# Performance work log

Measured on AMD Instinct MI355X. Metric: run time of the kernel, lower is better.

## Reference

```python
import jax, jax.numpy as jnp
import numpy as np

N, IN, HID, HEADS, FFN = 2048, 768, 1024, 8, 2048
NH = HID // HEADS  # 128 per-head hidden


def setup_inputs() -> dict:
    key = jax.random.key(0)
    ks = jax.random.split(key, 24)
    s = 0.02
    inp = {
        "feature": jax.random.normal(ks[0], (1, N, IN), jnp.float32),
        "adj": jax.random.bernoulli(ks[1], 0.05, (1, N, N)).astype(jnp.float32),
        "gat1_W1": jax.random.normal(ks[2], (IN, HID), jnp.float32) * s,
        "gat1_a1": jax.random.normal(ks[3], (2 * NH,), jnp.float32) * s,
        "gat1_W2": jax.random.normal(ks[4], (HID, IN), jnp.float32) * s,
        "gat1_a2": jax.random.normal(ks[5], (2 * IN,), jnp.float32) * s,
        "gat2_W1": jax.random.normal(ks[6], (IN, HID), jnp.float32) * s,
        "gat2_a1": jax.random.normal(ks[7], (2 * NH,), jnp.float32) * s,
        "gat2_W2": jax.random.normal(ks[8], (HID, IN), jnp.float32) * s,
        "gat2_a2": jax.random.normal(ks[9], (2 * IN,), jnp.float32) * s,
        "Wf": jax.random.normal(ks[10], (2 * IN, IN), jnp.float32) * s,
        "bf": jnp.zeros((IN,), jnp.float32),
        "ffn_W1": jax.random.normal(ks[11], (IN, FFN), jnp.float32) * s,
        "ffn_b1": jnp.zeros((FFN,), jnp.float32),
        "ffn_W2": jax.random.normal(ks[12], (FFN, FFN), jnp.float32) * s,
        "ffn_b2": jnp.zeros((FFN,), jnp.float32),
        "ffn_W3": jax.random.normal(ks[13], (FFN, IN), jnp.float32) * s,
        "ffn_b3": jnp.zeros((IN,), jnp.float32),
        "out_W1": jax.random.normal(ks[14], (IN, FFN), jnp.float32) * s,
        "out_b1": jnp.zeros((FFN,), jnp.float32),
        "out_W2": jax.random.normal(ks[15], (FFN, IN), jnp.float32) * s,
        "out_b2": jnp.zeros((IN,), jnp.float32),
    }
    return inp


def leaky(x, slope):
    return jnp.where(x >= 0, x, slope * x)


def gat_layer(h, adjb, W, a, heads, concat):
    # h: [N, F_in]; adjb: [N, N] bool. Scores decompose since attn weight is
    # shared across heads: e_ij = leaky(a_l . g_i + a_r . g_j).
    n = h.shape[0]
    g = (h @ W).reshape(n, heads, -1)           # [N, H, F']
    f = g.shape[-1]
    gl = jnp.einsum("nhf,f->nh", g, a[:f])
    gr = jnp.einsum("nhf,f->nh", g, a[f:])
    e = leaky(gl[:, None, :] + gr[None, :, :], 0.2)   # [N, N, H]
    e = jnp.where(adjb[:, :, None], e, jnp.float32(-1e9))
    att = jax.nn.softmax(e, axis=1)             # softmax over source j
    out = jnp.einsum("ijh,jhf->ihf", att, g)    # [N, H, F']
    return out.reshape(n, -1) if concat else out.mean(axis=1)


def gat(x, adj2d, W1, a1, W2, a2):
    adjb = adj2d != 0
    x1 = jax.nn.elu(gat_layer(x, adjb, W1, a1, HEADS, True))
    return gat_layer(x1, adjb, W2, a2, 1, False)


def reference(feature, adj, gat1_W1, gat1_a1, gat1_W2, gat1_a2,
              gat2_W1, gat2_a1, gat2_W2, gat2_a2, Wf, bf,
              ffn_W1, ffn_b1, ffn_W2, ffn_b2, ffn_W3, ffn_b3,
              out_W1, out_b1, out_W2, out_b2):
    sen_adj = adj.at[:, :, -6:].set(0.0)
    sec_adj = jnp.zeros_like(adj).at[:, :, -6:].set(adj[:, :, -6:])
    x = feature[0]                               # [N, IN]
    f_sen = gat(x, sen_adj[0], gat1_W1, gat1_a1, gat1_W2, gat1_a2) + x
    f_sec = gat(x, sec_adj[0], gat2_W1, gat2_a1, gat2_W2, gat2_a2) + x
    f = jnp.concatenate([f_sec, f_sen], axis=-1)
    f = leaky(f @ Wf + bf, 0.01)                 # fusion linear + leaky
    # ffn: MLP(layers=3, keep_last=False) -> act on every layer
    f = leaky(f @ ffn_W1 + ffn_b1, 0.01)
    f = leaky(f @ ffn_W2 + ffn_b2, 0.01)
    f = leaky(f @ ffn_W3 + ffn_b3, 0.01)
    # out_ffn: MLP(layers=2)
    o = leaky(f @ out_W1 + out_b1, 0.01)
    o = leaky(o @ out_W2 + out_b2, 0.01)
    return (o + x)[None]                         # residual, [1, N, IN]
```

## Files before the change

### kernel.cpp

```cpp
#include <hip/hip_runtime.h>
#include <hip/hip_bf16.h>
#include <cmath>

#define NN 2048
#define DIN 768
#define DHID 1024
#define NHEADS 8
#define FPRIME 128
#define DFFN 2048
#define SEN_LIM 2042
#define MAXDEG 256

using short8 = __attribute__((ext_vector_type(8))) short;
using f32x4  = __attribute__((ext_vector_type(4))) float;

#if defined(__has_builtin)
#  if __has_builtin(__builtin_amdgcn_global_load_lds)
#    define HAVE_GLL 1
#  endif
#endif
#ifndef HAVE_GLL
#  define HAVE_GLL 0
#endif

__device__ inline unsigned short f2bf(float f) {
    unsigned u = __float_as_uint(f);
    unsigned r = u + 0x7FFFu + ((u >> 16) & 1u);
    return (unsigned short)(r >> 16);
}
__device__ inline float bf2f(unsigned short h) {
    return __uint_as_float(((unsigned)h) << 16);
}
__device__ inline void store_out(float* p, float v) { *p = v; }
__device__ inline void store_out(unsigned short* p, float v) { *p = f2bf(v); }

#if HAVE_GLL
__device__ inline void gll16(const unsigned short* g, unsigned short* l) {
    __builtin_amdgcn_global_load_lds(
        (const __attribute__((address_space(1))) unsigned int*)g,
        (__attribute__((address_space(3))) unsigned int*)l, 16, 0, 0);
}
#endif

__global__ __launch_bounds__(256) void build_nbrs(
    const float* __restrict__ adj,
    unsigned short* __restrict__ sen_idx, int* __restrict__ sen_cnt,
    unsigned short* __restrict__ sec_idx, int* __restrict__ sec_cnt)
{
    const int i = blockIdx.x;
    __shared__ int c_sen, c_sec;
    if (threadIdx.x == 0) { c_sen = 0; c_sec = 0; }
    __syncthreads();
    for (int j4 = threadIdx.x; j4 < NN / 4; j4 += 256) {
        float4 v = *(const float4*)&adj[(size_t)i * NN + j4 * 4];
        float vs[4] = {v.x, v.y, v.z, v.w};
        #pragma unroll
        for (int q = 0; q < 4; ++q) {
            if (vs[q] != 0.0f) {
                int j = j4 * 4 + q;
                if (j < SEN_LIM) {
                    int p = atomicAdd(&c_sen, 1);
                    if (p < MAXDEG) sen_idx[(size_t)i * MAXDEG + p] = (unsigned short)j;
                } else {
                    int p = atomicAdd(&c_sec, 1);
                    if (p < 8) sec_idx[i * 8 + p] = (unsigned short)j;
                }
            }
        }
    }
    __syncthreads();
    if (threadIdx.x == 0) { sen_cnt[i] = min(c_sen, MAXDEG); sec_cnt[i] = min(c_sec, 8); }
}

__global__ __launch_bounds__(256) void transpose_cast(
    const float* __restrict__ W, unsigned short* __restrict__ WT, int K, int N)
{
    __shared__ float t[32][33];
    const int bn = blockIdx.x * 32, bk = blockIdx.y * 32;
    const int tx = threadIdx.x & 31, ty = threadIdx.x >> 5;
    #pragma unroll
    for (int r = 0; r < 4; ++r)
        t[ty + r * 8][tx] = W[(size_t)(bk + ty + r * 8) * N + bn + tx];
    __syncthreads();
    #pragma unroll
    for (int r = 0; r < 4; ++r) {
        int n = ty + r * 8;
        WT[(size_t)(bn + n) * K + bk + tx] = f2bf(t[tx][n]);
    }
}

__global__ __launch_bounds__(256) void cast_bf16(
    const float* __restrict__ in, unsigned short* __restrict__ out, int n)
{
    int t = blockIdx.x * 256 + threadIdx.x;
    if (t < n) out[t] = f2bf(in[t]);
}

__global__ __launch_bounds__(256) void zero_f32(float* p, int n)
{
    int t = blockIdx.x * 256 + threadIdx.x;
    if (t < n) p[t] = 0.f;
}

__global__ __launch_bounds__(256) void col_mean(
    const float* __restrict__ g, int C, float* __restrict__ out)
{
    int c = blockIdx.x * 256 + threadIdx.x;
    int r0 = blockIdx.y * 128;
    float s = 0.f;
    for (int r = r0; r < r0 + 128; ++r) s += g[(size_t)r * C + c];
    atomicAdd(&out[c], s * (1.0f / 2048.0f));
}

template<int BM, int BN, typename OUT_T>
__global__ __launch_bounds__(256) void gemm_mfma(
    const unsigned short* __restrict__ A, const unsigned short* __restrict__ BT,
    const float* __restrict__ bias, const float* __restrict__ resid,
    OUT_T* __restrict__ C, unsigned short* __restrict__ Cb,
    int M, int N, int K, int act)
{
    constexpr int BK = 64;
    constexpr int WR = BM / 64;
    constexpr int WC = 4 / WR;
    constexpr int NF = BN / (WC * 16);
    constexpr int ACH = BM / 32;
    constexpr int BCH = BN / 32;
    __shared__ unsigned short Asm[BM * BK];
    __shared__ unsigned short Bsm[BN * BK];
    const int tid = threadIdx.x;
    const int lane = tid & 63, w = tid >> 6;
    const int wr = w / WC, wc = w % WC;
    const int bm = blockIdx.y * BM, bn = blockIdx.x * BN;

    f32x4 acc[4][NF];
    #pragma unroll
    for (int mi = 0; mi < 4; ++mi)
        #pragma unroll
        for (int ni = 0; ni < NF; ++ni)
            acc[mi][ni] = (f32x4){0.f, 0.f, 0.f, 0.f};

    const unsigned short* Abase = A + (size_t)bm * K;
    const unsigned short* Bbase = BT + (size_t)bn * K;

    for (int k0 = 0; k0 < K; k0 += BK) {
        __syncthreads();
        #pragma unroll
        for (int c = 0; c < ACH; ++c) {
            int e = (tid + c * 256) * 8;
            int r = e >> 6, kk = e & 63;
            int kks = kk ^ ((r & 7) << 3);
#if HAVE_GLL
            gll16(&Abase[(size_t)r * K + k0 + kks], &Asm[e]);
#else
            *(short8*)&Asm[e] = *(const short8*)&Abase[(size_t)r * K + k0 + kks];
#endif
        }
        #pragma unroll
        for (int c = 0; c < BCH; ++c) {
            int e = (tid + c * 256) * 8;
            int r = e >> 6, kk = e & 63;
            int kks = kk ^ ((r & 7) << 3);
#if HAVE_GLL
            gll16(&Bbase[(size_t)r * K + k0 + kks], &Bsm[e]);
#else
            *(short8*)&Bsm[e] = *(const short8*)&Bbase[(size_t)r * K + k0 + kks];
#endif
        }
        __syncthreads();
        #pragma unroll
        for (int ks = 0; ks < 2; ++ks) {
            short8 af[4], bfv[NF];
            #pragma unroll
            for (int mi = 0; mi < 4; ++mi) {
                int row = wr * 64 + mi * 16 + (lane & 15);
                int col = (ks * 32 + (lane >> 4) * 8) ^ ((row & 7) << 3);
                af[mi] = *(const short8*)&Asm[row * 64 + col];
            }
            #pragma unroll
            for (int ni = 0; ni < NF; ++ni) {
                int row = wc * (BN / WC) + ni * 16 + (lane & 15);
                int col = (ks * 32 + (lane >> 4) * 8) ^ ((row & 7) << 3);
                bfv[ni] = *(const short8*)&Bsm[row * 64 + col];
            }
            #pragma unroll
            for (int mi = 0; mi < 4; ++mi)
                #pragma unroll
                for (int ni = 0; ni < NF; ++ni)
                    acc[mi][ni] = __builtin_amdgcn_mfma_f32_16x16x32_bf16(
                        af[mi], bfv[ni], acc[mi][ni], 0, 0, 0);
        }
    }

    const int rbase = bm + wr * 64;
    const int cbase = bn + wc * (BN / WC);
    #pragma unroll
    for (int mi = 0; mi < 4; ++mi)
        #pragma unroll
        for (int ni = 0; ni < NF; ++ni)
            #pragma unroll
            for (int r = 0; r < 4; ++r) {
                int grow = rbase + mi * 16 + (lane >> 4) * 4 + r;
                int gcol = cbase + ni * 16 + (lane & 15);
                float v = acc[mi][ni][r];
                if (bias)  v += bias[gcol];
                if (act)   v = (v >= 0.f) ? v : 0.01f * v;
                if (resid) v += resid[(size_t)grow * N + gcol];
                store_out(&C[(size_t)grow * N + gcol], v);
                if (Cb) Cb[(size_t)grow * N + gcol] = f2bf(v);
            }
}

__global__ __launch_bounds__(64) void glgr_kernel(
    const float* __restrict__ g, const float* __restrict__ a,
    int F, float* __restrict__ gl, float* __restrict__ gr)
{
    const int b = blockIdx.x;
    const int lane = threadIdx.x;
    const float* gb = g + (size_t)b * F;
    float sl = 0.f, sr = 0.f;
    for (int f = lane; f < F; f += 64) {
        float v = gb[f];
        sl += v * a[f];
        sr += v * a[F + f];
    }
    #pragma unroll
    for (int off = 32; off > 0; off >>= 1) {
        sl += __shfl_down(sl, off);
        sr += __shfl_down(sr, off);
    }
    if (lane == 0) { gl[b] = sl; gr[b] = sr; }
}

template<int H, int F, typename OUT_T>
__global__ __launch_bounds__(256) void attn_agg(
    const float* __restrict__ g,
    const unsigned short* __restrict__ gb,
    const float* __restrict__ gl,
    const float* __restrict__ gr,
    const unsigned short* __restrict__ idx, int idx_stride,
    const int* __restrict__ cnt,
    const float* __restrict__ gmean,
    OUT_T* __restrict__ dst, int dst_stride, int dst_coloff,
    const float* __restrict__ resid, int mode)
{
    constexpr int HF = H * F;
    const int i = blockIdx.x;
    const int tid = threadIdx.x;
    const int lane = tid & 63, w = tid >> 6;
    const int n = cnt[i];

    if (n == 0) {
        for (int c = tid; c < HF; c += 256) {
            float v = gmean[c];
            if (mode == 0) v = (v > 0.f) ? v : expm1f(v);
            else           v += resid[(size_t)i * HF + c];
            store_out(&dst[(size_t)i * dst_stride + dst_coloff + c], v);
        }
        return;
    }

    __shared__ float s_wred[4 * H];
    __shared__ float s_max[H], s_inv[H], s_glh[H];
    __shared__ float s_w[128 * H];
    __shared__ unsigned short s_j[128];

    if (tid < H) s_glh[tid] = gl[(size_t)i * H + tid];
    __syncthreads();
    float glh[H];
    #pragma unroll
    for (int h = 0; h < H; ++h) glh[h] = s_glh[h];

    const unsigned short* row_idx = idx + (size_t)i * idx_stride;

    float pmax[H];
    #pragma unroll
    for (int h = 0; h < H; ++h) pmax[h] = -1e30f;
    for (int jj = tid; jj < n; jj += 256) {
        int j = row_idx[jj];
        if (H == 8) {
            float4 ga = *(const float4*)&gr[(size_t)j * 8];
            float4 gbv = *(const float4*)&gr[(size_t)j * 8 + 4];
            float sc[8] = {ga.x, ga.y, ga.z, ga.w, gbv.x, gbv.y, gbv.z, gbv.w};
            #pragma unroll
            for (int h = 0; h < H; ++h) {
                float s = glh[h] + sc[h];
                s = (s >= 0.f) ? s : 0.2f * s;
                pmax[h] = fmaxf(pmax[h], s);
            }
        } else {
            float s = glh[0] + gr[j];
            s = (s >= 0.f) ? s : 0.2f * s;
            pmax[0] = fmaxf(pmax[0], s);
        }
    }
    #pragma unroll
    for (int h = 0; h < H; ++h)
        #pragma unroll
        for (int off = 32; off > 0; off >>= 1)
            pmax[h] = fmaxf(pmax[h], __shfl_xor(pmax[h], off));
    if (lane == 0)
        #pragma unroll
        for (int h = 0; h < H; ++h) s_wred[w * H + h] = pmax[h];
    __syncthreads();
    if (tid < H)
        s_max[tid] = fmaxf(fmaxf(s_wred[tid], s_wred[H + tid]),
                           fmaxf(s_wred[2 * H + tid], s_wred[3 * H + tid]));
    __syncthreads();
    float mx[H];
    #pragma unroll
    for (int h = 0; h < H; ++h) mx[h] = s_max[h];

    float psum[H];
    #pragma unroll
    for (int h = 0; h < H; ++h) psum[h] = 0.f;
    for (int jj = tid; jj < n; jj += 256) {
        int j = row_idx[jj];
        if (H == 8) {
            float4 ga = *(const float4*)&gr[(size_t)j * 8];
            float4 gbv = *(const float4*)&gr[(size_t)j * 8 + 4];
            float sc[8] = {ga.x, ga.y, ga.z, ga.w, gbv.x, gbv.y, gbv.z, gbv.w};
            #pragma unroll
            for (int h = 0; h < H; ++h) {
                float s = glh[h] + sc[h];
                s = (s >= 0.f) ? s : 0.2f * s;
                psum[h] += expf(s - mx[h]);
            }
        } else {
            float s = glh[0] + gr[j];
            s = (s >= 0.f) ? s : 0.2f * s;
            psum[0] += expf(s - mx[0]);
        }
    }
    #pragma unroll
    for (int h = 0; h < H; ++h)
        #pragma unroll
        for (int off = 32; off > 0; off >>= 1)
            psum[h] += __shfl_xor(psum[h], off);
    if (lane == 0)
        #pragma unroll
        for (int h = 0; h < H; ++h) s_wred[w * H + h] = psum[h];
    __syncthreads();
    if (tid < H)
        s_inv[tid] = 1.f / (s_wred[tid] + s_wred[H + tid] +
                            s_wred[2 * H + tid] + s_wred[3 * H + tid]);

    const int cb = tid * 4;
    const bool active = (cb < HF);
    const int hh = (H == 8) ? (cb >> 7) : 0;
    float a0 = 0.f, a1 = 0.f, a2 = 0.f, a3 = 0.f;

    for (int c0 = 0; c0 < n; c0 += 128) {
        int m = min(128, n - c0);
        __syncthreads();
        for (int e = tid; e < m * H; e += 256) {
            int jj = (H == 8) ? (e >> 3) : e;
            int h  = (H == 8) ? (e & 7) : 0;
            int j = row_idx[c0 + jj];
            float s = glh[h] + gr[(size_t)j * H + h];
            s = (s >= 0.f) ? s : 0.2f * s;
            s_w[jj * H + h] = expf(s - s_max[h]) * s_inv[h];
            if (h == 0) s_j[jj] = (unsigned short)j;
        }
        __syncthreads();
        if (active) {
            int jj = 0;
            for (; jj + 4 <= m; jj += 4) {
                ushort4 v0 = *(const ushort4*)&gb[(size_t)s_j[jj]     * HF + cb];
                ushort4 v1 = *(const ushort4*)&gb[(size_t)s_j[jj + 1] * HF + cb];
                ushort4 v2 = *(const ushort4*)&gb[(size_t)s_j[jj + 2] * HF + cb];
                ushort4 v3 = *(const ushort4*)&gb[(size_t)s_j[jj + 3] * HF + cb];
                float w0 = s_w[jj * H + hh], w1 = s_w[(jj + 1) * H + hh];
                float w2 = s_w[(jj + 2) * H + hh], w3 = s_w[(jj + 3) * H + hh];
                a0 += w0 * bf2f(v0.x) + w1 * bf2f(v1.x) + w2 * bf2f(v2.x) + w3 * bf2f(v3.x);
                a1 += w0 * bf2f(v0.y) + w1 * bf2f(v1.y) + w2 * bf2f(v2.y) + w3 * bf2f(v3.y);
                a2 += w0 * bf2f(v0.z) + w1 * bf2f(v1.z) + w2 * bf2f(v2.z) + w3 * bf2f(v3.z);
                a3 += w0 * bf2f(v0.w) + w1 * bf2f(v1.w) + w2 * bf2f(v2.w) + w3 * bf2f(v3.w);
            }
            for (; jj < m; ++jj) {
                ushort4 v0 = *(const ushort4*)&gb[(size_t)s_j[jj] * HF + cb];
                float w0 = s_w[jj * H + hh];
                a0 += w0 * bf2f(v0.x); a1 += w0 * bf2f(v0.y);
                a2 += w0 * bf2f(v0.z); a3 += w0 * bf2f(v0.w);
            }
        }
    }

    if (active) {
        float vv[4] = {a0, a1, a2, a3};
        #pragma unroll
        for (int q = 0; q < 4; ++q) {
            float v = vv[q];
            if (mode == 0) v = (v > 0.f) ? v : expm1f(v);
            else           v += resid[(size_t)i * HF + cb + q];
            store_out(&dst[(size_t)i * dst_stride + dst_coloff + cb + q], v);
        }
    }
}

extern "C" void kernel_launch(void* const* d_in, const int* in_sizes, int n_in,
                              void* d_out, int out_size, void* d_ws, size_t ws_size,
                              hipStream_t stream)
{
    const float* feature = (const float*)d_in[0];
    const float* adj     = (const float*)d_in[1];
    const float* g1W1 = (const float*)d_in[2];
    const float* g1a1 = (const float*)d_in[3];
    const float* g1W2 = (const float*)d_in[4];
    const float* g1a2 = (const float*)d_in[5];
    const float* g2W1 = (const float*)d_in[6];
    const float* g2a1 = (const float*)d_in[7];
    const float* g2W2 = (const float*)d_in[8];
    const float* g2a2 = (const float*)d_in[9];
    const float* Wf  = (const float*)d_in[10];
    const float* bfv = (const float*)d_in[11];
    const float* fW1 = (const float*)d_in[12];
    const float* fb1 = (const float*)d_in[13];
    const float* fW2 = (const float*)d_in[14];
    const float* fb2 = (const float*)d_in[15];
    const float* fW3 = (const float*)d_in[16];
    const float* fb3 = (const float*)d_in[17];
    const float* oW1 = (const float*)d_in[18];
    const float* ob1 = (const float*)d_in[19];
    const float* oW2 = (const float*)d_in[20];
    const float* ob2 = (const float*)d_in[21];
    float* out = (float*)d_out;

    char* ws = (char*)d_ws;
    size_t off = 0;
    auto alloc = [&](size_t bytes) -> void* {
        void* p = ws + off;
        off = (off + bytes + 255) & ~(size_t)255;
        return p;
    };
    typedef unsigned short bf_t;
    int* sen_cnt = (int*)alloc((size_t)NN * 4);
    int* sec_cnt = (int*)alloc((size_t)NN * 4);
    unsigned short* sen_idx = (unsigned short*)alloc((size_t)NN * MAXDEG * 2);
    unsigned short* sec_idx = (unsigned short*)alloc((size_t)NN * 8 * 2);
    float* g1buf = (float*)alloc((size_t)NN * DHID * 4);
    bf_t*  g1b   = (bf_t*)alloc((size_t)NN * DHID * 2);
    float* gl1   = (float*)alloc((size_t)NN * NHEADS * 4);
    float* gr1   = (float*)alloc((size_t)NN * NHEADS * 4);
    bf_t*  x1    = (bf_t*)alloc((size_t)NN * DHID * 2);
    float* g2buf = (float*)alloc((size_t)NN * DIN * 4);
    bf_t*  g2b   = (bf_t*)alloc((size_t)NN * DIN * 2);
    float* gl2   = (float*)alloc((size_t)NN * 4);
    float* gr2   = (float*)alloc((size_t)NN * 4);
    float* gmean = (float*)alloc((size_t)DHID * 4);
    bf_t*  fcat  = (bf_t*)alloc((size_t)NN * (2 * DIN) * 2);
    bf_t*  fbuf  = (bf_t*)alloc((size_t)NN * DIN * 2);
    bf_t*  tA    = (bf_t*)alloc((size_t)NN * DFFN * 2);
    bf_t*  tB    = (bf_t*)alloc((size_t)NN * DFFN * 2);
    bf_t*  featb = (bf_t*)alloc((size_t)NN * DIN * 2);
    bf_t* g1W1T = (bf_t*)alloc((size_t)DIN * DHID * 2);
    bf_t* g1W2T = (bf_t*)alloc((size_t)DHID * DIN * 2);
    bf_t* g2W1T = (bf_t*)alloc((size_t)DIN * DHID * 2);
    bf_t* g2W2T = (bf_t*)alloc((size_t)DHID * DIN * 2);
    bf_t* WfT   = (bf_t*)alloc((size_t)(2 * DIN) * DIN * 2);
    bf_t* fW1T  = (bf_t*)alloc((size_t)DIN * DFFN * 2);
    bf_t* fW2T  = (bf_t*)alloc((size_t)DFFN * DFFN * 2);
    bf_t* fW3T  = (bf_t*)alloc((size_t)DFFN * DIN * 2);
    bf_t* oW1T  = (bf_t*)alloc((size_t)DIN * DFFN * 2);
    bf_t* oW2T  = (bf_t*)alloc((size_t)DFFN * DIN * 2);

    build_nbrs<<<NN, 256, 0, stream>>>(adj, sen_idx, sen_cnt, sec_idx, sec_cnt);
    auto tp = [&](const float* W, bf_t* WT, int K, int N) {
        transpose_cast<<<dim3(N / 32, K / 32), 256, 0, stream>>>(W, WT, K, N);
    };
    tp(g1W1, g1W1T, DIN, DHID);   tp(g1W2, g1W2T, DHID, DIN);
    tp(g2W1, g2W1T, DIN, DHID);   tp(g2W2, g2W2T, DHID, DIN);
    tp(Wf, WfT, 2 * DIN, DIN);
    tp(fW1, fW1T, DIN, DFFN);     tp(fW2, fW2T, DFFN, DFFN);
    tp(fW3, fW3T, DFFN, DIN);
    tp(oW1, oW1T, DIN, DFFN);     tp(oW2, oW2T, DFFN, DIN);
    cast_bf16<<<(NN * DIN) / 256, 256, 0, stream>>>(feature, featb, NN * DIN);

    auto run_gat = [&](const bf_t* W1T, const float* a1, const bf_t* W2T, const float* a2,
                       const unsigned short* idx, int idx_stride, const int* cnt, int coloff) {
        gemm_mfma<64, 64, float><<<dim3(DHID / 64, NN / 64), 256, 0, stream>>>(
            featb, W1T, nullptr, nullptr, g1buf, g1b, NN, DHID, DIN, 0);
        glgr_kernel<<<NN * NHEADS, 64, 0, stream>>>(g1buf, a1, FPRIME, gl1, gr1);
        zero_f32<<<DHID / 256, 256, 0, stream>>>(gmean, DHID);
        col_mean<<<dim3(DHID / 256, 16), 256, 0, stream>>>(g1buf, DHID, gmean);
        attn_agg<NHEADS, FPRIME, bf_t><<<NN, 256, 0, stream>>>(
            g1buf, g1b, gl1, gr1, idx, idx_stride, cnt, gmean, x1, DHID, 0, nullptr, 0);
        gemm_mfma<64, 64, float><<<dim3(DIN / 64, NN / 64), 256, 0, stream>>>(
            x1, W2T, nullptr, nullptr, g2buf, g2b, NN, DIN, DHID, 0);
        glgr_kernel<<<NN, 64, 0, stream>>>(g2buf, a2, DIN, gl2, gr2);
        zero_f32<<<DIN / 256, 256, 0, stream>>>(gmean, DIN);
        col_mean<<<dim3(DIN / 256, 16), 256, 0, stream>>>(g2buf, DIN, gmean);
        attn_agg<1, DIN, bf_t><<<NN, 256, 0, stream>>>(
            g2buf, g2b, gl2, gr2, idx, idx_stride, cnt, gmean, fcat, 2 * DIN, coloff, feature, 1);
    };

    run_gat(g1W1T, g1a1, g1W2T, g1a2, sen_idx, MAXDEG, sen_cnt, DIN);
    run_gat(g2W1T, g2a1, g2W2T, g2a2, sec_idx, 8, sec_cnt, 0);

    gemm_mfma<64, 64, bf_t><<<dim3(DIN / 64, NN / 64), 256, 0, stream>>>(
        fcat, WfT, bfv, nullptr, fbuf, nullptr, NN, DIN, 2 * DIN, 1);
    gemm_mfma<64, 128, bf_t><<<dim3(DFFN / 128, NN / 64), 256, 0, stream>>>(
        fbuf, fW1T, fb1, nullptr, tA, nullptr, NN, DFFN, DIN, 1);
    gemm_mfma<64, 128, bf_t><<<dim3(DFFN / 128, NN / 64), 256, 0, stream>>>(
        tA, fW2T, fb2, nullptr, tB, nullptr, NN, DFFN, DFFN, 1);
    gemm_mfma<64, 64, bf_t><<<dim3(DIN / 64, NN / 64), 256, 0, stream>>>(
        tB, fW3T, fb3, nullptr, fbuf, nullptr, NN, DIN, DFFN, 1);
    gemm_mfma<64, 128, bf_t><<<dim3(DFFN / 128, NN / 64), 256, 0, stream>>>(
        fbuf, oW1T, ob1, nullptr, tA, nullptr, NN, DFFN, DIN, 1);
    gemm_mfma<64, 64, float><<<dim3(DIN / 64, NN / 64), 256, 0, stream>>>(
        tA, oW2T, ob2, feature, out, nullptr, NN, DIN, DFFN, 1);
}
```

Before: 522.2 us.

## Batch both GAT branches into shared launches and merge weight preprocessing

Merges all weight transposes and the feature cast into a single job-table kernel. It concatenates the two first-layer GAT weights into one wider GEMM, and runs the second-layer GEMM, score, column-mean and aggregation kernels for both branches in one launch each via a branch index. Intermediate projections are kept in bf16 only, which removes the fp32 copies and halves traffic for scores and means. The aggregation inner loop is unrolled to 8 neighbors. The aim is to cut launch count and fill the GPU better for the tiny second branch, at the cost of reading scores and means from bf16-rounded values.

```diff
diff --git a/kernel.cpp b/kernel.cpp
--- a/kernel.cpp
+++ b/kernel.cpp
@@ -72,51 +72,47 @@
     if (threadIdx.x == 0) { sen_cnt[i] = min(c_sen, MAXDEG); sec_cnt[i] = min(c_sec, 8); }
 }
 
-__global__ __launch_bounds__(256) void transpose_cast(
-    const float* __restrict__ W, unsigned short* __restrict__ WT, int K, int N)
+struct TPJob { const float* s; unsigned short* d; int K, N, start, trans; };
+struct TPJobs { TPJob j[11]; };
+
+__global__ __launch_bounds__(256) void mega_tp(TPJobs jobs, int njobs)
 {
     __shared__ float t[32][33];
-    const int bn = blockIdx.x * 32, bk = blockIdx.y * 32;
+    const int tile = blockIdx.x;
+    int ji = 0;
+    for (int k = 1; k < 11; ++k)
+        if (k < njobs && tile >= jobs.j[k].start) ji = k;
+    const TPJob jb = jobs.j[ji];
+    const int lt = tile - jb.start;
+    const int ntx = jb.N >> 5;
+    const int bn = (lt % ntx) * 32, bk = (lt / ntx) * 32;
     const int tx = threadIdx.x & 31, ty = threadIdx.x >> 5;
-    #pragma unroll
-    for (int r = 0; r < 4; ++r)
-        t[ty + r * 8][tx] = W[(size_t)(bk + ty + r * 8) * N + bn + tx];
-    __syncthreads();
-    #pragma unroll
-    for (int r = 0; r < 4; ++r) {
-        int n = ty + r * 8;
-        WT[(size_t)(bn + n) * K + bk + tx] = f2bf(t[tx][n]);
-    }
-}
-
-__global__ __launch_bounds__(256) void cast_bf16(
-    const float* __restrict__ in, unsigned short* __restrict__ out, int n)
-{
-    int t = blockIdx.x * 256 + threadIdx.x;
-    if (t < n) out[t] = f2bf(in[t]);
-}
-
-__global__ __launch_bounds__(256) void zero_f32(float* p, int n)
-{
-    int t = blockIdx.x * 256 + threadIdx.x;
-    if (t < n) p[t] = 0.f;
-}
-
-__global__ __launch_bounds__(256) void col_mean(
-    const float* __restrict__ g, int C, float* __restrict__ out)
-{
-    int c = blockIdx.x * 256 + threadIdx.x;
-    int r0 = blockIdx.y * 128;
-    float s = 0.f;
-    for (int r = r0; r < r0 + 128; ++r) s += g[(size_t)r * C + c];
-    atomicAdd(&out[c], s * (1.0f / 2048.0f));
+    if (jb.trans) {
+        #pragma unroll
+        for (int r = 0; r < 4; ++r)
+            t[ty + r * 8][tx] = jb.s[(size_t)(bk + ty + r * 8) * jb.N + bn + tx];
+        __syncthreads();
+        #pragma unroll
+        for (int r = 0; r < 4; ++r) {
+            int n = ty + r * 8;
+            jb.d[(size_t)(bn + n) * jb.K + bk + tx] = f2bf(t[tx][n]);
+        }
+    } else {
+        #pragma unroll
+        for (int r = 0; r < 4; ++r) {
+            size_t e = (size_t)(bk + ty + r * 8) * jb.N + bn + tx;
+            jb.d[e] = f2bf(jb.s[e]);
+        }
+    }
 }
 
 template<int BM, int BN, typename OUT_T>
 __global__ __launch_bounds__(256) void gemm_mfma(
-    const unsigned short* __restrict__ A, const unsigned short* __restrict__ BT,
+    const unsigned short* __restrict__ A0, const unsigned short* __restrict__ A1,
+    const unsigned short* __restrict__ BT0, const unsigned short* __restrict__ BT1,
     const float* __restrict__ bias, const float* __restrict__ resid,
-    OUT_T* __restrict__ C, unsigned short* __restrict__ Cb,
+    OUT_T* __restrict__ C0, OUT_T* __restrict__ C1,
+    unsigned short* __restrict__ Cb0, unsigned short* __restrict__ Cb1,
     int M, int N, int K, int act)
 {
     constexpr int BK = 64;
@@ -127,6 +123,11 @@
     constexpr int BCH = BN / 32;
     __shared__ unsigned short Asm[BM * BK];
     __shared__ unsigned short Bsm[BN * BK];
+    const int z = blockIdx.z;
+    const unsigned short* A  = z ? A1  : A0;
+    const unsigned short* BT = z ? BT1 : BT0;
+    OUT_T* C = z ? C1 : C0;
+    unsigned short* Cb = z ? Cb1 : Cb0;
     const int tid = threadIdx.x;
     const int lane = tid & 63, w = tid >> 6;
     const int wr = w / WC, wc = w % WC;
@@ -210,16 +211,24 @@
             }
 }
 
-__global__ __launch_bounds__(64) void glgr_kernel(
-    const float* __restrict__ g, const float* __restrict__ a,
-    int F, float* __restrict__ gl, float* __restrict__ gr)
-{
-    const int b = blockIdx.x;
-    const int lane = threadIdx.x;
-    const float* gb = g + (size_t)b * F;
+__global__ __launch_bounds__(64) void glgr2(
+    const unsigned short* __restrict__ gA, const unsigned short* __restrict__ gB,
+    int row_stride, int F, int Hlog2, int nb_per_branch,
+    const float* __restrict__ aA, const float* __restrict__ aB,
+    float* __restrict__ glA, float* __restrict__ grA,
+    float* __restrict__ glB, float* __restrict__ grB,
+    float* __restrict__ z, int zblocks)
+{
+    const int bid = blockIdx.x, lane = threadIdx.x;
+    if (bid < zblocks) z[bid * 64 + lane] = 0.f;
+    const int br = bid >= nb_per_branch;
+    const int b = br ? bid - nb_per_branch : bid;
+    const int node = b >> Hlog2, h = b - ((b >> Hlog2) << Hlog2);
+    const unsigned short* g = (br ? gB : gA) + (size_t)node * row_stride + h * F;
+    const float* a = br ? aB : aA;
     float sl = 0.f, sr = 0.f;
     for (int f = lane; f < F; f += 64) {
-        float v = gb[f];
+        float v = bf2f(g[f]);
         sl += v * a[f];
         sr += v * a[F + f];
     }
@@ -228,23 +237,52 @@
         sl += __shfl_down(sl, off);
         sr += __shfl_down(sr, off);
     }
-    if (lane == 0) { gl[b] = sl; gr[b] = sr; }
+    if (lane == 0) {
+        (br ? glB : glA)[b] = sl;
+        (br ? grB : grA)[b] = sr;
+    }
+}
+
+__global__ __launch_bounds__(256) void col_mean2(
+    const unsigned short* __restrict__ g0, const unsigned short* __restrict__ g1,
+    int C, float* __restrict__ o0, float* __restrict__ o1)
+{
+    const unsigned short* g = blockIdx.z ? g1 : g0;
+    float* o = blockIdx.z ? o1 : o0;
+    int c = blockIdx.x * 256 + threadIdx.x;
+    int r0 = blockIdx.y * 128;
+    float s = 0.f;
+    for (int r = r0; r < r0 + 128; ++r) s += bf2f(g[(size_t)r * C + c]);
+    atomicAdd(&o[c], s * (1.0f / 2048.0f));
 }
 
 template<int H, int F, typename OUT_T>
-__global__ __launch_bounds__(256) void attn_agg(
-    const float* __restrict__ g,
-    const unsigned short* __restrict__ gb,
-    const float* __restrict__ gl,
-    const float* __restrict__ gr,
-    const unsigned short* __restrict__ idx, int idx_stride,
-    const int* __restrict__ cnt,
-    const float* __restrict__ gmean,
-    OUT_T* __restrict__ dst, int dst_stride, int dst_coloff,
+__global__ __launch_bounds__(256) void attn_agg2(
+    const unsigned short* __restrict__ gb0, const unsigned short* __restrict__ gb1,
+    int g_stride,
+    const float* __restrict__ gl0, const float* __restrict__ gr0,
+    const float* __restrict__ gl1, const float* __restrict__ gr1,
+    const unsigned short* __restrict__ idx0, int is0, const int* __restrict__ cnt0,
+    const unsigned short* __restrict__ idx1, int is1, const int* __restrict__ cnt1,
+    const float* __restrict__ gmean0, const float* __restrict__ gmean1,
+    OUT_T* __restrict__ dst0, OUT_T* __restrict__ dst1,
+    int dst_stride, int co0, int co1,
     const float* __restrict__ resid, int mode)
 {
     constexpr int HF = H * F;
-    const int i = blockIdx.x;
+    const int bid = blockIdx.x;
+    const int br = bid >= NN;
+    const int i = br ? bid - NN : bid;
+    const unsigned short* gbp = br ? gb1 : gb0;
+    const float* gl = br ? gl1 : gl0;
+    const float* gr = br ? gr1 : gr0;
+    const unsigned short* idx = br ? idx1 : idx0;
+    const int is = br ? is1 : is0;
+    const int* cnt = br ? cnt1 : cnt0;
+    const float* gmean = br ? gmean1 : gmean0;
+    OUT_T* dst = br ? dst1 : dst0;
+    const int co = br ? co1 : co0;
+
     const int tid = threadIdx.x;
     const int lane = tid & 63, w = tid >> 6;
     const int n = cnt[i];
@@ -254,7 +292,7 @@
             float v = gmean[c];
             if (mode == 0) v = (v > 0.f) ? v : expm1f(v);
             else           v += resid[(size_t)i * HF + c];
-            store_out(&dst[(size_t)i * dst_stride + dst_coloff + c], v);
+            store_out(&dst[(size_t)i * dst_stride + co + c], v);
         }
         return;
     }
@@ -270,7 +308,7 @@
     #pragma unroll
     for (int h = 0; h < H; ++h) glh[h] = s_glh[h];
 
-    const unsigned short* row_idx = idx + (size_t)i * idx_stride;
+    const unsigned short* row_idx = idx + (size_t)i * is;
 
     float pmax[H];
     #pragma unroll
@@ -364,20 +402,23 @@
         __syncthreads();
         if (active) {
             int jj = 0;
-            for (; jj + 4 <= m; jj += 4) {
-                ushort4 v0 = *(const ushort4*)&gb[(size_t)s_j[jj]     * HF + cb];
-                ushort4 v1 = *(const ushort4*)&gb[(size_t)s_j[jj + 1] * HF + cb];
-                ushort4 v2 = *(const ushort4*)&gb[(size_t)s_j[jj + 2] * HF + cb];
-                ushort4 v3 = *(const ushort4*)&gb[(size_t)s_j[jj + 3] * HF + cb];
-                float w0 = s_w[jj * H + hh], w1 = s_w[(jj + 1) * H + hh];
-                float w2 = s_w[(jj + 2) * H + hh], w3 = s_w[(jj + 3) * H + hh];
-                a0 += w0 * bf2f(v0.x) + w1 * bf2f(v1.x) + w2 * bf2f(v2.x) + w3 * bf2f(v3.x);
-                a1 += w0 * bf2f(v0.y) + w1 * bf2f(v1.y) + w2 * bf2f(v2.y) + w3 * bf2f(v3.y);
-                a2 += w0 * bf2f(v0.z) + w1 * bf2f(v1.z) + w2 * bf2f(v2.z) + w3 * bf2f(v3.z);
-                a3 += w0 * bf2f(v0.w) + w1 * bf2f(v1.w) + w2 * bf2f(v2.w) + w3 * bf2f(v3.w);
+            for (; jj + 8 <= m; jj += 8) {
+                ushort4 v[8]; float wv[8];
+                #pragma unroll
+                for (int u = 0; u < 8; ++u) {
+                    v[u] = *(const ushort4*)&gbp[(size_t)s_j[jj + u] * g_stride + cb];
+                    wv[u] = s_w[(jj + u) * H + hh];
+                }
+                #pragma unroll
+                for (int u = 0; u < 8; ++u) {
+                    a0 += wv[u] * bf2f(v[u].x);
+                    a1 += wv[u] * bf2f(v[u].y);
+                    a2 += wv[u] * bf2f(v[u].z);
+                    a3 += wv[u] * bf2f(v[u].w);
+                }
             }
             for (; jj < m; ++jj) {
-                ushort4 v0 = *(const ushort4*)&gb[(size_t)s_j[jj] * HF + cb];
+                ushort4 v0 = *(const ushort4*)&gbp[(size_t)s_j[jj] * g_stride + cb];
                 float w0 = s_w[jj * H + hh];
                 a0 += w0 * bf2f(v0.x); a1 += w0 * bf2f(v0.y);
                 a2 += w0 * bf2f(v0.z); a3 += w0 * bf2f(v0.w);
@@ -392,7 +433,7 @@
             float v = vv[q];
             if (mode == 0) v = (v > 0.f) ? v : expm1f(v);
             else           v += resid[(size_t)i * HF + cb + q];
-            store_out(&dst[(size_t)i * dst_stride + dst_coloff + cb + q], v);
+            store_out(&dst[(size_t)i * dst_stride + co + cb + q], v);
         }
     }
 }
@@ -437,24 +478,28 @@
     int* sec_cnt = (int*)alloc((size_t)NN * 4);
     unsigned short* sen_idx = (unsigned short*)alloc((size_t)NN * MAXDEG * 2);
     unsigned short* sec_idx = (unsigned short*)alloc((size_t)NN * 8 * 2);
-    float* g1buf = (float*)alloc((size_t)NN * DHID * 4);
-    bf_t*  g1b   = (bf_t*)alloc((size_t)NN * DHID * 2);
-    float* gl1   = (float*)alloc((size_t)NN * NHEADS * 4);
-    float* gr1   = (float*)alloc((size_t)NN * NHEADS * 4);
-    bf_t*  x1    = (bf_t*)alloc((size_t)NN * DHID * 2);
-    float* g2buf = (float*)alloc((size_t)NN * DIN * 4);
-    bf_t*  g2b   = (bf_t*)alloc((size_t)NN * DIN * 2);
-    float* gl2   = (float*)alloc((size_t)NN * 4);
-    float* gr2   = (float*)alloc((size_t)NN * 4);
-    float* gmean = (float*)alloc((size_t)DHID * 4);
+    bf_t*  g1b   = (bf_t*)alloc((size_t)NN * 2048 * 2);
+    float* gl1a  = (float*)alloc((size_t)NN * NHEADS * 4);
+    float* gr1a  = (float*)alloc((size_t)NN * NHEADS * 4);
+    float* gl1b  = (float*)alloc((size_t)NN * NHEADS * 4);
+    float* gr1b  = (float*)alloc((size_t)NN * NHEADS * 4);
+    bf_t*  x1a   = (bf_t*)alloc((size_t)NN * DHID * 2);
+    bf_t*  x1b   = (bf_t*)alloc((size_t)NN * DHID * 2);
+    bf_t*  g2aB  = (bf_t*)alloc((size_t)NN * DIN * 2);
+    bf_t*  g2bB  = (bf_t*)alloc((size_t)NN * DIN * 2);
+    float* gl2a  = (float*)alloc((size_t)NN * 4);
+    float* gr2a  = (float*)alloc((size_t)NN * 4);
+    float* gl2b  = (float*)alloc((size_t)NN * 4);
+    float* gr2b  = (float*)alloc((size_t)NN * 4);
+    float* gmeanL1 = (float*)alloc((size_t)2048 * 4);
+    float* gmeanL2 = (float*)alloc((size_t)1536 * 4);
     bf_t*  fcat  = (bf_t*)alloc((size_t)NN * (2 * DIN) * 2);
     bf_t*  fbuf  = (bf_t*)alloc((size_t)NN * DIN * 2);
     bf_t*  tA    = (bf_t*)alloc((size_t)NN * DFFN * 2);
     bf_t*  tB    = (bf_t*)alloc((size_t)NN * DFFN * 2);
     bf_t*  featb = (bf_t*)alloc((size_t)NN * DIN * 2);
-    bf_t* g1W1T = (bf_t*)alloc((size_t)DIN * DHID * 2);
+    bf_t* W1T_AB = (bf_t*)alloc((size_t)2048 * DIN * 2);
     bf_t* g1W2T = (bf_t*)alloc((size_t)DHID * DIN * 2);
-    bf_t* g2W1T = (bf_t*)alloc((size_t)DIN * DHID * 2);
     bf_t* g2W2T = (bf_t*)alloc((size_t)DHID * DIN * 2);
     bf_t* WfT   = (bf_t*)alloc((size_t)(2 * DIN) * DIN * 2);
     bf_t* fW1T  = (bf_t*)alloc((size_t)DIN * DFFN * 2);
@@ -464,48 +509,75 @@
     bf_t* oW2T  = (bf_t*)alloc((size_t)DFFN * DIN * 2);
 
     build_nbrs<<<NN, 256, 0, stream>>>(adj, sen_idx, sen_cnt, sec_idx, sec_cnt);
-    auto tp = [&](const float* W, bf_t* WT, int K, int N) {
-        transpose_cast<<<dim3(N / 32, K / 32), 256, 0, stream>>>(W, WT, K, N);
+
+    TPJobs jobs;
+    int cur = 0, nj = 0;
+    auto addjob = [&](const float* s, bf_t* d, int K, int N, int trans) {
+        jobs.j[nj] = {s, d, K, N, cur, trans};
+        cur += (K / 32) * (N / 32);
+        ++nj;
     };
-    tp(g1W1, g1W1T, DIN, DHID);   tp(g1W2, g1W2T, DHID, DIN);
-    tp(g2W1, g2W1T, DIN, DHID);   tp(g2W2, g2W2T, DHID, DIN);
-    tp(Wf, WfT, 2 * DIN, DIN);
-    tp(fW1, fW1T, DIN, DFFN);     tp(fW2, fW2T, DFFN, DFFN);
-    tp(fW3, fW3T, DFFN, DIN);
-    tp(oW1, oW1T, DIN, DFFN);     tp(oW2, oW2T, DFFN, DIN);
-    cast_bf16<<<(NN * DIN) / 256, 256, 0, stream>>>(feature, featb, NN * DIN);
-
-    auto run_gat = [&](const bf_t* W1T, const float* a1, const bf_t* W2T, const float* a2,
-                       const unsigned short* idx, int idx_stride, const int* cnt, int coloff) {
-        gemm_mfma<64, 64, float><<<dim3(DHID / 64, NN / 64), 256, 0, stream>>>(
-            featb, W1T, nullptr, nullptr, g1buf, g1b, NN, DHID, DIN, 0);
-        glgr_kernel<<<NN * NHEADS, 64, 0, stream>>>(g1buf, a1, FPRIME, gl1, gr1);
-        zero_f32<<<DHID / 256, 256, 0, stream>>>(gmean, DHID);
-        col_mean<<<dim3(DHID / 256, 16), 256, 0, stream>>>(g1buf, DHID, gmean);
-        attn_agg<NHEADS, FPRIME, bf_t><<<NN, 256, 0, stream>>>(
-            g1buf, g1b, gl1, gr1, idx, idx_stride, cnt, gmean, x1, DHID, 0, nullptr, 0);
-        gemm_mfma<64, 64, float><<<dim3(DIN / 64, NN / 64), 256, 0, stream>>>(
-            x1, W2T, nullptr, nullptr, g2buf, g2b, NN, DIN, DHID, 0);
-        glgr_kernel<<<NN, 64, 0, stream>>>(g2buf, a2, DIN, gl2, gr2);
-        zero_f32<<<DIN / 256, 256, 0, stream>>>(gmean, DIN);
-        col_mean<<<dim3(DIN / 256, 16), 256, 0, stream>>>(g2buf, DIN, gmean);
-        attn_agg<1, DIN, bf_t><<<NN, 256, 0, stream>>>(
-            g2buf, g2b, gl2, gr2, idx, idx_stride, cnt, gmean, fcat, 2 * DIN, coloff, feature, 1);
-    };
-
-    run_gat(g1W1T, g1a1, g1W2T, g1a2, sen_idx, MAXDEG, sen_cnt, DIN);
-    run_gat(g2W1T, g2a1, g2W2T, g2a2, sec_idx, 8, sec_cnt, 0);
-
-    gemm_mfma<64, 64, bf_t><<<dim3(DIN / 64, NN / 64), 256, 0, stream>>>(
-        fcat, WfT, bfv, nullptr, fbuf, nullptr, NN, DIN, 2 * DIN, 1);
-    gemm_mfma<64, 128, bf_t><<<dim3(DFFN / 128, NN / 64), 256, 0, stream>>>(
-        fbuf, fW1T, fb1, nullptr, tA, nullptr, NN, DFFN, DIN, 1);
-    gemm_mfma<64, 128, bf_t><<<dim3(DFFN / 128, NN / 64), 256, 0, stream>>>(
-        tA, fW2T, fb2, nullptr, tB, nullptr, NN, DFFN, DFFN, 1);
-    gemm_mfma<64, 64, bf_t><<<dim3(DIN / 64, NN / 64), 256, 0, stream>>>(
-        tB, fW3T, fb3, nullptr, fbuf, nullptr, NN, DIN, DFFN, 1);
-    gemm_mfma<64, 128, bf_t><<<dim3(DFFN / 128, NN / 64), 256, 0, stream>>>(
-        fbuf, oW1T, ob1, nullptr, tA, nullptr, NN, DFFN, DIN, 1);
-    gemm_mfma<64, 64, float><<<dim3(DIN / 64, NN / 64), 256, 0, stream>>>(
-        tA, oW2T, ob2, feature, out, nullptr, NN, DIN, DFFN, 1);
-}
+    addjob(g1W1, W1T_AB, DIN, DHID, 1);
+    addjob(g2W1, W1T_AB + (size_t)1024 * DIN, DIN, DHID, 1);
+    addjob(g1W2, g1W2T, DHID, DIN, 1);
+    addjob(g2W2, g2W2T, DHID, DIN, 1);
+    addjob(Wf, WfT, 2 * DIN, DIN, 1);
+    addjob(fW1, fW1T, DIN, DFFN, 1);
+    addjob(fW2, fW2T, DFFN, DFFN, 1);
+    addjob(fW3, fW3T, DFFN, DIN, 1);
+    addjob(oW1, oW1T, DIN, DFFN, 1);
+    addjob(oW2, oW2T, DFFN, DIN, 1);
+    addjob(feature, featb, NN, DIN, 0);
+    mega_tp<<<cur, 256, 0, stream>>>(jobs, nj);
+
+    gemm_mfma<64, 128, bf_t><<<dim3(2048 / 128, NN / 64, 1), 256, 0, stream>>>(
+        featb, nullptr, W1T_AB, nullptr, nullptr, nullptr,
+        g1b, nullptr, nullptr, nullptr, NN, 2048, DIN, 0);
+
+    glgr2<<<2 * NN * NHEADS, 64, 0, stream>>>(
+        g1b, g1b + 1024, 2048, FPRIME, 3, NN * NHEADS,
+        g1a1, g2a1, gl1a, gr1a, gl1b, gr1b, gmeanL1, 32);
+    col_mean2<<<dim3(2048 / 256, 16, 1), 256, 0, stream>>>(
+        g1b, nullptr, 2048, gmeanL1, nullptr);
+    attn_agg2<NHEADS, FPRIME, bf_t><<<2 * NN, 256, 0, stream>>>(
+        g1b, g1b + 1024, 2048,
+        gl1a, gr1a, gl1b, gr1b,
+        sen_idx, MAXDEG, sen_cnt, sec_idx, 8, sec_cnt,
+        gmeanL1, gmeanL1 + 1024,
+        x1a, x1b, DHID, 0, 0, nullptr, 0);
+
+    gemm_mfma<64, 64, bf_t><<<dim3(DIN / 64, NN / 64, 2), 256, 0, stream>>>(
+        x1a, x1b, g1W2T, g2W2T, nullptr, nullptr,
+        g2aB, g2bB, nullptr, nullptr, NN, DIN, DHID, 0);
+
+    glgr2<<<2 * NN, 64, 0, stream>>>(
+        g2aB, g2bB, DIN, DIN, 0, NN,
+        g1a2, g2a2, gl2a, gr2a, gl2b, gr2b, gmeanL2, 24);
+    col_mean2<<<dim3(DIN / 256, 16, 2), 256, 0, stream>>>(
+        g2aB, g2bB, DIN, gmeanL2, gmeanL2 + DIN);
+    attn_agg2<1, DIN, bf_t><<<2 * NN, 256, 0, stream>>>(
+        g2aB, g2bB, DIN,
+        gl2a, gr2a, gl2b, gr2b,
+        sen_idx, MAXDEG, sen_cnt, sec_idx, 8, sec_cnt,
+        gmeanL2, gmeanL2 + DIN,
+        fcat, fcat, 2 * DIN, DIN, 0, feature, 1);
+
+    gemm_mfma<64, 64, bf_t><<<dim3(DIN / 64, NN / 64, 1), 256, 0, stream>>>(
+        fcat, nullptr, WfT, nullptr, bfv, nullptr,
+        fbuf, nullptr, nullptr, nullptr, NN, DIN, 2 * DIN, 1);
+    gemm_mfma<64, 128, bf_t><<<dim3(DFFN / 128, NN / 64, 1), 256, 0, stream>>>(
+        fbuf, nullptr, fW1T, nullptr, fb1, nullptr,
+        tA, nullptr, nullptr, nullptr, NN, DFFN, DIN, 1);
+    gemm_mfma<64, 128, bf_t><<<dim3(DFFN / 128, NN / 64, 1), 256, 0, stream>>>(
+        tA, nullptr, fW2T, nullptr, fb2, nullptr,
+        tB, nullptr, nullptr, nullptr, NN, DFFN, DFFN, 1);
+    gemm_mfma<64, 64, bf_t><<<dim3(DIN / 64, NN / 64, 1), 256, 0, stream>>>(
+        tB, nullptr, fW3T, nullptr, fb3, nullptr,
+        fbuf, nullptr, nullptr, nullptr, NN, DIN, DFFN, 1);
+    gemm_mfma<64, 128, bf_t><<<dim3(DFFN / 128, NN / 64, 1), 256, 0, stream>>>(
+        fbuf, nullptr, oW1T, nullptr, ob1, nullptr,
+        tA, nullptr, nullptr, nullptr, NN, DFFN, DIN, 1);
+    gemm_mfma<64, 64, float><<<dim3(DIN / 64, NN / 64, 1), 256, 0, stream>>>(
+        tA, nullptr, oW2T, nullptr, ob2, feature,
+        out, nullptr, nullptr, nullptr, NN, DIN, DFFN, 1);
+}
```

After: 447.3 us. 14.3% less time.
